# Kernel tuning notes

Measured on AMD Instinct MI355X. Metric: run time of the kernel, lower is better.

The kernel has to match this reference:

```python
import jax, jax.numpy as jnp
import numpy as np

N = 50000
H = 256
EPS = 1e-5

def setup_inputs() -> dict:
    key = jax.random.key(0)
    ks = jax.random.split(key, 8)
    d = 128
    inp = {
        'x': jax.random.normal(ks[0], (N, d), jnp.float32),
        'edge_index': jax.random.randint(ks[1], (2, 800000), 0, N, jnp.int64),
        'W1': jax.random.normal(ks[2], (d, H), jnp.float32) * (2.0 / d) ** 0.5,
        'b1': jnp.zeros((H,), jnp.float32),
        'g1': jnp.ones((H,), jnp.float32),
        'be1': jnp.zeros((H,), jnp.float32),
        'W2': jax.random.normal(ks[3], (H, H), jnp.float32) * (2.0 / H) ** 0.5,
        'b2': jnp.zeros((H,), jnp.float32),
        'g2': jnp.ones((H,), jnp.float32),
        'be2': jnp.zeros((H,), jnp.float32),
        'W3': jax.random.normal(ks[4], (H, H), jnp.float32) * (2.0 / H) ** 0.5,
        'b3': jnp.zeros((H,), jnp.float32),
        'g3': jnp.ones((H,), jnp.float32),
        'be3': jnp.zeros((H,), jnp.float32),
        'Wf1': jax.random.normal(ks[5], (H, H // 2), jnp.float32) * (2.0 / H) ** 0.5,
        'bf1': jnp.zeros((H // 2,), jnp.float32),
        'Wf2': jax.random.normal(ks[6], (H // 2, 1), jnp.float32) * (2.0 / (H // 2)) ** 0.5,
        'bf2': jnp.zeros((1,), jnp.float32),
    }
    return inp

def _gcn_norm(edge_index):
    # add self-loops, symmetric normalization (PyG GCNConv defaults)
    loop = jnp.arange(N, dtype=edge_index.dtype)
    row = jnp.concatenate([edge_index[0], loop])  # source
    col = jnp.concatenate([edge_index[1], loop])  # target
    deg = jax.ops.segment_sum(jnp.ones_like(col, jnp.float32), col, num_segments=N)
    dis = jnp.where(deg > 0, jax.lax.rsqrt(deg), 0.0)
    norm = dis[row] * dis[col]  # [E+N]
    return row, col, norm

def _conv(x, W, b, row, col, norm):
    xw = x @ W                       # [N,H]
    msg = xw[row] * norm[:, None]    # gather + scale, [E+N,H]
    out = jax.ops.segment_sum(msg, col, num_segments=N)
    return out + b

def _ln(x, g, b):
    mu = jnp.mean(x, axis=-1, keepdims=True)
    var = jnp.var(x, axis=-1, keepdims=True)
    return (x - mu) * jax.lax.rsqrt(var + EPS) * g + b

def reference(x, edge_index, W1, b1, g1, be1, W2, b2, g2, be2, W3, b3, g3, be3, Wf1, bf1, Wf2, bf2):
    row, col, norm = _gcn_norm(edge_index)
    x1 = jax.nn.relu(_ln(_conv(x, W1, b1, row, col, norm), g1, be1))
    x2 = jax.nn.relu(_ln(_conv(x1, W2, b2, row, col, norm), g2, be2)) + 0.7 * x1
    x3 = jax.nn.relu(_ln(_conv(x2, W3, b3, row, col, norm), g3, be3)) * 0.7 + x2
    h = jax.nn.relu(x3 @ Wf1 + bf1)
    return h @ Wf2 + bf2  # [N,1]
```

## Files before the change

### kernel.cpp

```cpp
#include <hip/hip_runtime.h>
#include <cstdint>
#include <cstddef>

#define HDIM 256
#define DIN 128
#define EPSV 1e-5f
#define SCHUNK 1024

typedef __attribute__((ext_vector_type(8))) short short8;
typedef __attribute__((ext_vector_type(4))) float f32x4;

__device__ __forceinline__ float bf2f(unsigned int u16) {
  union { unsigned int i; float f; } v; v.i = u16 << 16; return v.f;
}
__device__ __forceinline__ unsigned short f2bf(float f) {
  union { float f; unsigned int i; } v; v.f = f;
  unsigned int u = v.i;
  return (unsigned short)((u + 0x7fffu + ((u >> 16) & 1u)) >> 16);
}
__device__ __forceinline__ float4 ldbf4(const unsigned short* p) {
  uint2 v = *(const uint2*)p;
  return make_float4(bf2f(v.x & 0xffffu), bf2f(v.x >> 16),
                     bf2f(v.y & 0xffffu), bf2f(v.y >> 16));
}
__device__ __forceinline__ void stbf4(unsigned short* p, float a, float b, float c, float d) {
  uint2 o;
  o.x = (unsigned int)f2bf(a) | ((unsigned int)f2bf(b) << 16);
  o.y = (unsigned int)f2bf(c) | ((unsigned int)f2bf(d) << 16);
  *(uint2*)p = o;
}
#define ACC8(u) do { \
    acc[0] += bf2f((u).x & 0xffffu); acc[1] += bf2f((u).x >> 16); \
    acc[2] += bf2f((u).y & 0xffffu); acc[3] += bf2f((u).y >> 16); \
    acc[4] += bf2f((u).z & 0xffffu); acc[5] += bf2f((u).z >> 16); \
    acc[6] += bf2f((u).w & 0xffffu); acc[7] += bf2f((u).w >> 16); } while (0)

__global__ __launch_bounds__(256) void hist_k(const int* __restrict__ col, int* deg, int e) {
  int i = blockIdx.x * 256 + threadIdx.x;
  if (i < e) atomicAdd(&deg[col[i]], 1);
}

__global__ __launch_bounds__(256) void scanA_k(const int* __restrict__ deg,
                                               int* __restrict__ row_ptr,
                                               int* __restrict__ blockSums,
                                               float* __restrict__ dis, int n) {
  __shared__ int waveSums[4];
  const int tid = threadIdx.x, lane = tid & 63, w = tid >> 6;
  const int base = blockIdx.x * SCHUNK + tid * 4;
  int v0 = 0, v1 = 0, v2 = 0, v3 = 0;
  if (base + 0 < n) v0 = deg[base + 0];
  if (base + 1 < n) v1 = deg[base + 1];
  if (base + 2 < n) v2 = deg[base + 2];
  if (base + 3 < n) v3 = deg[base + 3];
  if (base + 0 < n) dis[base + 0] = rsqrtf((float)(v0 + 1));
  if (base + 1 < n) dis[base + 1] = rsqrtf((float)(v1 + 1));
  if (base + 2 < n) dis[base + 2] = rsqrtf((float)(v2 + 1));
  if (base + 3 < n) dis[base + 3] = rsqrtf((float)(v3 + 1));
  int tsum = v0 + v1 + v2 + v3;
  int inc = tsum;
#pragma unroll
  for (int off = 1; off < 64; off <<= 1) {
    int t = __shfl_up(inc, off);
    if (lane >= off) inc += t;
  }
  if (lane == 63) waveSums[w] = inc;
  __syncthreads();
  int woff = 0;
#pragma unroll
  for (int k = 0; k < 4; ++k) woff += (k < w) ? waveSums[k] : 0;
  int excl = woff + inc - tsum;
  if (base + 0 < n) row_ptr[base + 0] = excl;
  if (base + 1 < n) row_ptr[base + 1] = excl + v0;
  if (base + 2 < n) row_ptr[base + 2] = excl + v0 + v1;
  if (base + 3 < n) row_ptr[base + 3] = excl + v0 + v1 + v2;
  if (tid == 255) blockSums[blockIdx.x] = woff + inc;
}

__global__ __launch_bounds__(256) void scanC_k(int* __restrict__ row_ptr,
                                               const int* __restrict__ bsums,
                                               int n, int e, int nbs) {
  __shared__ int s_add;
  if (threadIdx.x < 64) {
    int v = (threadIdx.x < nbs && threadIdx.x < blockIdx.x) ? bsums[threadIdx.x] : 0;
#pragma unroll
    for (int off = 1; off < 64; off <<= 1) v += __shfl_xor(v, off);
    if (threadIdx.x == 0) s_add = v;
  }
  __syncthreads();
  const int add = s_add;
  const int base = blockIdx.x * SCHUNK + threadIdx.x * 4;
#pragma unroll
  for (int k = 0; k < 4; ++k)
    if (base + k < n) row_ptr[base + k] += add;
  if (blockIdx.x == 0 && threadIdx.x == 0) row_ptr[n] = e;
}

__global__ __launch_bounds__(256) void fill_k(const int* __restrict__ row,
                                              const int* __restrict__ col,
                                              const int* __restrict__ row_ptr,
                                              int* cur, int* srcs, int e) {
  int i = blockIdx.x * 256 + threadIdx.x;
  if (i < e) {
    int c = col[i];
    int p = row_ptr[c] + atomicAdd(&cur[c], 1);
    srcs[p] = row[i];
  }
}

__device__ __forceinline__ void packW(const float* __restrict__ W,
                                      unsigned short* __restrict__ out,
                                      int idx, int C) {
  int j = idx & 7, lane = (idx >> 3) & 63, rest = idx >> 9;
  int NSUB = C >> 4;
  int ns = rest % NSUB, kb = rest / NSUB;
  int k = kb * 32 + (lane >> 4) * 8 + j;
  int c = ns * 16 + (lane & 15);
  out[idx] = f2bf(W[(size_t)k * C + c]);
}

__global__ __launch_bounds__(256) void prep_k(
    const float* __restrict__ W1, const float* __restrict__ W2,
    const float* __restrict__ W3, const float* __restrict__ Wf1,
    const float* __restrict__ x, const float* __restrict__ dis,
    unsigned short* __restrict__ W1p, unsigned short* __restrict__ W2p,
    unsigned short* __restrict__ W3p, unsigned short* __restrict__ Wf1p,
    unsigned short* __restrict__ xs, int nx) {
  int idx = blockIdx.x * 256 + threadIdx.x;
  const int s0 = DIN * HDIM, s1 = s0 + HDIM * HDIM, s2 = s1 + HDIM * HDIM,
            s3 = s2 + HDIM * 128;
  if (idx < s0) packW(W1, W1p, idx, HDIM);
  else if (idx < s1) packW(W2, W2p, idx - s0, HDIM);
  else if (idx < s2) packW(W3, W3p, idx - s1, HDIM);
  else if (idx < s3) packW(Wf1, Wf1p, idx - s2, 128);
  else {
    int o = idx - s3;
    if (o < nx) xs[o] = f2bf(x[o] * dis[o >> 7]);
  }
}

template<int MODE, int K, bool SOUT>
__global__ __launch_bounds__(512) void fused_k(
    const unsigned short* __restrict__ xs, const int* __restrict__ row_ptr,
    const int* __restrict__ srcs, const float* __restrict__ dis,
    const unsigned short* __restrict__ Wp,
    const float* __restrict__ bias, const float* __restrict__ gam,
    const float* __restrict__ bet, const unsigned short* __restrict__ xprev,
    unsigned short* __restrict__ out, int n) {
  constexpr int CN = 256, NSUB = 16, KC = K / 32;
  constexpr int STRIDE = K + 8;
  constexpr int LPR = K / 8;
  constexpr int RP = 64 / LPR;
  constexpr int NIT = 8 / RP;
  __shared__ unsigned short aggS[64 * STRIDE];
  __shared__ float red_s[64][4], red_q[64][4];

  const int t = threadIdx.x;
  const int w = t >> 6, lane = t & 63;
  const int m0 = blockIdx.x * 64;

  {
    const int gi = lane / LPR, li = lane % LPR;
    const unsigned short* xb = xs + li * 8;
#pragma unroll
    for (int it = 0; it < NIT; ++it) {
      const int lr = w * 8 + it * RP + gi;
      const int tg = m0 + lr;
      const int tgc = tg < n ? tg : n - 1;
      const int beg = row_ptr[tgc], end = row_ptr[tgc + 1];
      const float di = dis[tgc];
      float acc[8];
      {
        uint4 v = *(const uint4*)(xb + (size_t)tgc * K);
        acc[0] = bf2f(v.x & 0xffffu); acc[1] = bf2f(v.x >> 16);
        acc[2] = bf2f(v.y & 0xffffu); acc[3] = bf2f(v.y >> 16);
        acc[4] = bf2f(v.z & 0xffffu); acc[5] = bf2f(v.z >> 16);
        acc[6] = bf2f(v.w & 0xffffu); acc[7] = bf2f(v.w >> 16);
      }
      int j = beg;
      for (; j + 16 <= end; j += 16) {
        int4 sA = *(const int4*)(srcs + j);
        int4 sB = *(const int4*)(srcs + j + 4);
        int4 sC = *(const int4*)(srcs + j + 8);
        int4 sD = *(const int4*)(srcs + j + 12);
        uint4 u0 = *(const uint4*)(xb + (size_t)sA.x * K);
        uint4 u1 = *(const uint4*)(xb + (size_t)sA.y * K);
        uint4 u2 = *(const uint4*)(xb + (size_t)sA.z * K);
        uint4 u3 = *(const uint4*)(xb + (size_t)sA.w * K);
        uint4 u4 = *(const uint4*)(xb + (size_t)sB.x * K);
        uint4 u5 = *(const uint4*)(xb + (size_t)sB.y * K);
        uint4 u6 = *(const uint4*)(xb + (size_t)sB.z * K);
        uint4 u7 = *(const uint4*)(xb + (size_t)sB.w * K);
        uint4 u8 = *(const uint4*)(xb + (size_t)sC.x * K);
        uint4 u9 = *(const uint4*)(xb + (size_t)sC.y * K);
        uint4 uA = *(const uint4*)(xb + (size_t)sC.z * K);
        uint4 uB = *(const uint4*)(xb + (size_t)sC.w * K);
        uint4 uC = *(const uint4*)(xb + (size_t)sD.x * K);
        uint4 uD = *(const uint4*)(xb + (size_t)sD.y * K);
        uint4 uE = *(const uint4*)(xb + (size_t)sD.z * K);
        uint4 uF = *(const uint4*)(xb + (size_t)sD.w * K);
        ACC8(u0); ACC8(u1); ACC8(u2); ACC8(u3);
        ACC8(u4); ACC8(u5); ACC8(u6); ACC8(u7);
        ACC8(u8); ACC8(u9); ACC8(uA); ACC8(uB);
        ACC8(uC); ACC8(uD); ACC8(uE); ACC8(uF);
      }
      for (; j + 4 <= end; j += 4) {
        int4 sA = *(const int4*)(srcs + j);
        uint4 u0 = *(const uint4*)(xb + (size_t)sA.x * K);
        uint4 u1 = *(const uint4*)(xb + (size_t)sA.y * K);
        uint4 u2 = *(const uint4*)(xb + (size_t)sA.z * K);
        uint4 u3 = *(const uint4*)(xb + (size_t)sA.w * K);
        ACC8(u0); ACC8(u1); ACC8(u2); ACC8(u3);
      }
      for (; j < end; ++j) {
        uint4 u = *(const uint4*)(xb + (size_t)srcs[j] * K);
        ACC8(u);
      }
      uint4 o;
      o.x = (unsigned int)f2bf(di * acc[0]) | ((unsigned int)f2bf(di * acc[1]) << 16);
      o.y = (unsigned int)f2bf(di * acc[2]) | ((unsigned int)f2bf(di * acc[3]) << 16);
      o.z = (unsigned int)f2bf(di * acc[4]) | ((unsigned int)f2bf(di * acc[5]) << 16);
      o.w = (unsigned int)f2bf(di * acc[6]) | ((unsigned int)f2bf(di * acc[7]) << 16);
      *(uint4*)&aggS[lr * STRIDE + li * 8] = o;
    }
  }
  __syncthreads();

  const int rg = w & 1, cg = w >> 1;
  const int gq = lane >> 4, i = lane & 15;
  const unsigned short* aL0 = &aggS[(rg * 32 + i) * STRIDE + gq * 8];
  const unsigned short* aL1 = aL0 + 16 * STRIDE;
  const short8* wp = (const short8*)Wp + (size_t)(cg * 4) * 64 + lane;

  f32x4 acc[2][4];
#pragma unroll
  for (int rr = 0; rr < 2; ++rr)
#pragma unroll
    for (int j = 0; j < 4; ++j) acc[rr][j] = (f32x4){0.f, 0.f, 0.f, 0.f};

  short8 wf[4];
#pragma unroll
  for (int j = 0; j < 4; ++j) wf[j] = wp[j * 64];

#pragma unroll
  for (int kc = 0; kc < KC; ++kc) {
    short8 nwf[4];
    if (kc + 1 < KC) {
#pragma unroll
      for (int j = 0; j < 4; ++j) nwf[j] = wp[(size_t)(kc + 1) * NSUB * 64 + j * 64];
    }
    short8 af0 = *(const short8*)(aL0 + kc * 32);
    short8 af1 = *(const short8*)(aL1 + kc * 32);
#pragma unroll
    for (int j = 0; j < 4; ++j) {
      acc[0][j] = __builtin_amdgcn_mfma_f32_16x16x32_bf16(wf[j], af0, acc[0][j], 0, 0, 0);
      acc[1][j] = __builtin_amdgcn_mfma_f32_16x16x32_bf16(wf[j], af1, acc[1][j], 0, 0, 0);
    }
    if (kc + 1 < KC) {
#pragma unroll
      for (int j = 0; j < 4; ++j) wf[j] = nwf[j];
    }
  }

  const int colb = cg * 64 + gq * 4;
  float s0 = 0.f, q0 = 0.f, s1 = 0.f, q1 = 0.f;
#pragma unroll
  for (int j = 0; j < 4; ++j) {
    f32x4 b4 = *(const f32x4*)(bias + colb + j * 16);
#pragma unroll
    for (int r = 0; r < 4; ++r) {
      acc[0][j][r] += b4[r];
      acc[1][j][r] += b4[r];
      float v = acc[0][j][r]; s0 += v; q0 += v * v;
      float u = acc[1][j][r]; s1 += u; q1 += u * u;
    }
  }
  s0 += __shfl_xor(s0, 16); s0 += __shfl_xor(s0, 32);
  q0 += __shfl_xor(q0, 16); q0 += __shfl_xor(q0, 32);
  s1 += __shfl_xor(s1, 16); s1 += __shfl_xor(s1, 32);
  q1 += __shfl_xor(q1, 16); q1 += __shfl_xor(q1, 32);
  if (gq == 0) {
    red_s[rg * 32 + i][cg] = s0;      red_q[rg * 32 + i][cg] = q0;
    red_s[rg * 32 + 16 + i][cg] = s1; red_q[rg * 32 + 16 + i][cg] = q1;
  }
  __syncthreads();

#pragma unroll
  for (int rr = 0; rr < 2; ++rr) {
    int il = rg * 32 + rr * 16 + i;
    int r = m0 + il;
    if (r >= n) continue;
    float ss = (red_s[il][0] + red_s[il][1]) + (red_s[il][2] + red_s[il][3]);
    float qq = (red_q[il][0] + red_q[il][1]) + (red_q[il][2] + red_q[il][3]);
    float mu = ss * (1.f / CN);
    float inv = rsqrtf(qq * (1.f / CN) - mu * mu + EPSV);
    float di = dis[r];
    float rinv = (MODE != 0) ? 1.0f / di : 0.f;
    unsigned short* op = out + (size_t)r * CN + colb;
    const unsigned short* pp = (MODE != 0) ? (xprev + (size_t)r * CN + colb) : nullptr;
#pragma unroll
    for (int j = 0; j < 4; ++j) {
      f32x4 g4 = *(const f32x4*)(gam + colb + j * 16);
      f32x4 e4 = *(const f32x4*)(bet + colb + j * 16);
      float o0 = fmaxf((acc[rr][j][0] - mu) * inv * g4[0] + e4[0], 0.f);
      float o1 = fmaxf((acc[rr][j][1] - mu) * inv * g4[1] + e4[1], 0.f);
      float o2 = fmaxf((acc[rr][j][2] - mu) * inv * g4[2] + e4[2], 0.f);
      float o3 = fmaxf((acc[rr][j][3] - mu) * inv * g4[3] + e4[3], 0.f);
      if (MODE == 1) {
        float4 pv = ldbf4(pp + j * 16);
        o0 += 0.7f * rinv * pv.x; o1 += 0.7f * rinv * pv.y;
        o2 += 0.7f * rinv * pv.z; o3 += 0.7f * rinv * pv.w;
      } else if (MODE == 2) {
        float4 pv = ldbf4(pp + j * 16);
        o0 = o0 * 0.7f + rinv * pv.x; o1 = o1 * 0.7f + rinv * pv.y;
        o2 = o2 * 0.7f + rinv * pv.z; o3 = o3 * 0.7f + rinv * pv.w;
      }
      if (SOUT) { o0 *= di; o1 *= di; o2 *= di; o3 *= di; }
      stbf4(op + j * 16, o0, o1, o2, o3);
    }
  }
}

__global__ __launch_bounds__(256) void gemmdot_k(
    const unsigned short* __restrict__ A, const unsigned short* __restrict__ Wp,
    const float* __restrict__ b1, const float* __restrict__ w2,
    const float* __restrict__ b2, float* __restrict__ out, int n) {
  constexpr int K = 256, NSUB = 8, KC = 8;
  __shared__ float redh[64][2];
  const int t = threadIdx.x;
  const int w = t >> 6, lane = t & 63;
  const int rg = w & 1, cg = w >> 1;
  const int gq = lane >> 4, i = lane & 15;
  const int m0 = blockIdx.x * 64;
  const int r0 = m0 + rg * 32 + i, r1 = r0 + 16;
  const int l0 = r0 < n ? r0 : n - 1, l1 = r1 < n ? r1 : n - 1;
  const unsigned short* a0 = A + (size_t)l0 * K + gq * 8;
  const unsigned short* a1 = A + (size_t)l1 * K + gq * 8;
  const short8* wp = (const short8*)Wp + (size_t)(cg * 4) * 64 + lane;

  f32x4 acc[2][4];
#pragma unroll
  for (int rr = 0; rr < 2; ++rr)
#pragma unroll
    for (int j = 0; j < 4; ++j) acc[rr][j] = (f32x4){0.f, 0.f, 0.f, 0.f};

  short8 af0 = *(const short8*)a0;
  short8 af1 = *(const short8*)a1;
  short8 wf[4];
#pragma unroll
  for (int j = 0; j < 4; ++j) wf[j] = wp[j * 64];

#pragma unroll
  for (int kc = 0; kc < KC; ++kc) {
    short8 naf0, naf1, nwf[4];
    if (kc + 1 < KC) {
      naf0 = *(const short8*)(a0 + (kc + 1) * 32);
      naf1 = *(const short8*)(a1 + (kc + 1) * 32);
#pragma unroll
      for (int j = 0; j < 4; ++j) nwf[j] = wp[(size_t)(kc + 1) * NSUB * 64 + j * 64];
    }
#pragma unroll
    for (int j = 0; j < 4; ++j) {
      acc[0][j] = __builtin_amdgcn_mfma_f32_16x16x32_bf16(wf[j], af0, acc[0][j], 0, 0, 0);
      acc[1][j] = __builtin_amdgcn_mfma_f32_16x16x32_bf16(wf[j], af1, acc[1][j], 0, 0, 0);
    }
    if (kc + 1 < KC) {
      af0 = naf0; af1 = naf1;
#pragma unroll
      for (int j = 0; j < 4; ++j) wf[j] = nwf[j];
    }
  }

  const int colb = cg * 64 + gq * 4;
  float p0 = 0.f, p1 = 0.f;
#pragma unroll
  for (int j = 0; j < 4; ++j) {
    f32x4 bb = *(const f32x4*)(b1 + colb + j * 16);
    f32x4 ww = *(const f32x4*)(w2 + colb + j * 16);
#pragma unroll
    for (int r = 0; r < 4; ++r) {
      p0 += fmaxf(acc[0][j][r] + bb[r], 0.f) * ww[r];
      p1 += fmaxf(acc[1][j][r] + bb[r], 0.f) * ww[r];
    }
  }
  p0 += __shfl_xor(p0, 16); p0 += __shfl_xor(p0, 32);
  p1 += __shfl_xor(p1, 16); p1 += __shfl_xor(p1, 32);
  if (gq == 0) {
    redh[rg * 32 + i][cg] = p0;
    redh[rg * 32 + 16 + i][cg] = p1;
  }
  __syncthreads();
  if (t < 64) {
    int r = m0 + t;
    if (r < n) out[r] = redh[t][0] + redh[t][1] + b2[0];
  }
}

extern "C" void kernel_launch(void* const* d_in, const int* in_sizes, int n_in,
                              void* d_out, int out_size, void* d_ws, size_t ws_size,
                              hipStream_t stream) {
  const float* x   = (const float*)d_in[0];
  const int*   ei  = (const int*)d_in[1];
  const float* W1  = (const float*)d_in[2];
  const float* b1  = (const float*)d_in[3];
  const float* g1  = (const float*)d_in[4];
  const float* be1 = (const float*)d_in[5];
  const float* W2  = (const float*)d_in[6];
  const float* b2  = (const float*)d_in[7];
  const float* g2  = (const float*)d_in[8];
  const float* be2 = (const float*)d_in[9];
  const float* W3  = (const float*)d_in[10];
  const float* b3  = (const float*)d_in[11];
  const float* g3  = (const float*)d_in[12];
  const float* be3 = (const float*)d_in[13];
  const float* Wf1 = (const float*)d_in[14];
  const float* bf1 = (const float*)d_in[15];
  const float* Wf2 = (const float*)d_in[16];
  const float* bf2 = (const float*)d_in[17];
  float* out = (float*)d_out;

  const int n = in_sizes[0] / DIN;
  const int e = in_sizes[1] / 2;
  const int* row = ei;
  const int* col = ei + e;

  char* ws = (char*)d_ws;
  size_t off = 0;
  auto alloc = [&](size_t bytes) -> void* {
    void* p = ws + off;
    off = (off + bytes + 255) & ~(size_t)255;
    return p;
  };
  float*          dis     = (float*)alloc((size_t)n * 4);
  int*            deg_i   = (int*)alloc((size_t)n * 4);
  int*            cur     = (int*)alloc((size_t)n * 4);
  int*            row_ptr = (int*)alloc((size_t)(n + 1) * 4);
  int*            bsums   = (int*)alloc((size_t)256 * 4);
  int*            srcs    = (int*)alloc((size_t)e * 4);
  unsigned short* W1p     = (unsigned short*)alloc((size_t)DIN * HDIM * 2);
  unsigned short* W2p     = (unsigned short*)alloc((size_t)HDIM * HDIM * 2);
  unsigned short* W3p     = (unsigned short*)alloc((size_t)HDIM * HDIM * 2);
  unsigned short* Wf1p    = (unsigned short*)alloc((size_t)HDIM * 128 * 2);
  unsigned short* xsb     = (unsigned short*)alloc((size_t)n * DIN * 2);
  unsigned short* x1s     = (unsigned short*)alloc((size_t)n * HDIM * 2);
  unsigned short* x2s     = (unsigned short*)alloc((size_t)n * HDIM * 2);
  unsigned short* x3      = (unsigned short*)alloc((size_t)n * HDIM * 2);

  const int eb  = (e + 255) / 256;
  const int gb  = (n + 63) / 64;
  const int sb_ = (n + SCHUNK - 1) / SCHUNK;
  const int prep_tot = DIN * HDIM + HDIM * HDIM + HDIM * HDIM + HDIM * 128 + n * DIN;

  hipMemsetAsync(deg_i, 0, ((char*)row_ptr - (char*)deg_i), stream);
  hist_k<<<eb, 256, 0, stream>>>(col, deg_i, e);
  scanA_k<<<sb_, 256, 0, stream>>>(deg_i, row_ptr, bsums, dis, n);
  scanC_k<<<sb_, 256, 0, stream>>>(row_ptr, bsums, n, e, sb_);
  fill_k<<<eb, 256, 0, stream>>>(row, col, row_ptr, cur, srcs, e);

  prep_k<<<(prep_tot + 255) / 256, 256, 0, stream>>>(W1, W2, W3, Wf1, x, dis,
                                                     W1p, W2p, W3p, Wf1p, xsb, n * DIN);

  fused_k<0, DIN, true><<<gb, 512, 0, stream>>>(
      xsb, row_ptr, srcs, dis, W1p, b1, g1, be1, nullptr, x1s, n);

  fused_k<1, HDIM, true><<<gb, 512, 0, stream>>>(
      x1s, row_ptr, srcs, dis, W2p, b2, g2, be2, x1s, x2s, n);

  fused_k<2, HDIM, false><<<gb, 512, 0, stream>>>(
      x2s, row_ptr, srcs, dis, W3p, b3, g3, be3, x2s, x3, n);

  gemmdot_k<<<gb, 256, 0, stream>>>(x3, Wf1p, bf1, Wf2, bf2, out, n);
}
```

Measured before the change: 480.4 us.

## Split GCN layers into gather and MFMA roles overlapped across half-graph launches

Each fused layer becomes two roles, an aggregation (gather) role that writes bf16 aggregates to a global buffer and a GEMM+LayerNorm role working on 128-row tiles. Rows are split into two halves and three launches are issued per layer, so gathering the second half runs alongside the GEMM on the first half. The aim is to overlap the memory-bound gather with MFMA work and to make GEMM tiles wider. CSR fill now reuses per-edge ranks from the histogram atomics instead of a second atomic pass, and the final GEMM-dot kernel moves to 512 threads and 128 rows per block. This costs a global round-trip for the aggregates, extra launches, and a larger workspace.

```diff
diff --git a/kernel.cpp b/kernel.cpp
--- a/kernel.cpp
+++ b/kernel.cpp
@@ -35,9 +35,10 @@
     acc[4] += bf2f((u).z & 0xffffu); acc[5] += bf2f((u).z >> 16); \
     acc[6] += bf2f((u).w & 0xffffu); acc[7] += bf2f((u).w >> 16); } while (0)
 
-__global__ __launch_bounds__(256) void hist_k(const int* __restrict__ col, int* deg, int e) {
+__global__ __launch_bounds__(256) void hist_k(const int* __restrict__ col,
+                                              int* deg, int* __restrict__ rank, int e) {
   int i = blockIdx.x * 256 + threadIdx.x;
-  if (i < e) atomicAdd(&deg[col[i]], 1);
+  if (i < e) rank[i] = atomicAdd(&deg[col[i]], 1);
 }
 
 __global__ __launch_bounds__(256) void scanA_k(const int* __restrict__ deg,
@@ -98,13 +99,10 @@
 __global__ __launch_bounds__(256) void fill_k(const int* __restrict__ row,
                                               const int* __restrict__ col,
                                               const int* __restrict__ row_ptr,
-                                              int* cur, int* srcs, int e) {
+                                              const int* __restrict__ rank,
+                                              int* __restrict__ srcs, int e) {
   int i = blockIdx.x * 256 + threadIdx.x;
-  if (i < e) {
-    int c = col[i];
-    int p = row_ptr[c] + atomicAdd(&cur[c], 1);
-    srcs[p] = row[i];
-  }
+  if (i < e) srcs[row_ptr[col[i]] + rank[i]] = row[i];
 }
 
 __device__ __forceinline__ void packW(const float* __restrict__ W,
@@ -139,132 +137,137 @@
 }
 
 template<int MODE, int K, bool SOUT>
-__global__ __launch_bounds__(512) void fused_k(
+__global__ __launch_bounds__(512) void combo_k(
     const unsigned short* __restrict__ xs, const int* __restrict__ row_ptr,
     const int* __restrict__ srcs, const float* __restrict__ dis,
-    const unsigned short* __restrict__ Wp,
+    unsigned short* __restrict__ agg, const unsigned short* __restrict__ Wp,
     const float* __restrict__ bias, const float* __restrict__ gam,
     const float* __restrict__ bet, const unsigned short* __restrict__ xprev,
-    unsigned short* __restrict__ out, int n) {
-  constexpr int CN = 256, NSUB = 16, KC = K / 32;
-  constexpr int STRIDE = K + 8;
-  constexpr int LPR = K / 8;
-  constexpr int RP = 64 / LPR;
-  constexpr int NIT = 8 / RP;
-  __shared__ unsigned short aggS[64 * STRIDE];
-  __shared__ float red_s[64][4], red_q[64][4];
-
+    unsigned short* __restrict__ out,
+    int Gb, int gRow0, int gEnd, int Lb, int lRow0, int lEnd, int n) {
+  constexpr int CN = 256, NSUBT = 16, KC = K / 32;
+  constexpr int LPR = K / 8, RPW = 64 / LPR, RPB = 8 * RPW;
+  __shared__ float red_s[128][2], red_q[128][2];
+  int b = blockIdx.x, role, sub;
+  int mm = 2 * (Gb < Lb ? Gb : Lb);
+  if (b < mm) { role = b & 1; sub = b >> 1; }
+  else { sub = (mm >> 1) + (b - mm); role = (Gb > Lb) ? 0 : 1; }
   const int t = threadIdx.x;
   const int w = t >> 6, lane = t & 63;
-  const int m0 = blockIdx.x * 64;
-
-  {
-    const int gi = lane / LPR, li = lane % LPR;
-    const unsigned short* xb = xs + li * 8;
-#pragma unroll
-    for (int it = 0; it < NIT; ++it) {
-      const int lr = w * 8 + it * RP + gi;
-      const int tg = m0 + lr;
-      const int tgc = tg < n ? tg : n - 1;
-      const int beg = row_ptr[tgc], end = row_ptr[tgc + 1];
-      const float di = dis[tgc];
-      float acc[8];
-      {
-        uint4 v = *(const uint4*)(xb + (size_t)tgc * K);
-        acc[0] = bf2f(v.x & 0xffffu); acc[1] = bf2f(v.x >> 16);
-        acc[2] = bf2f(v.y & 0xffffu); acc[3] = bf2f(v.y >> 16);
-        acc[4] = bf2f(v.z & 0xffffu); acc[5] = bf2f(v.z >> 16);
-        acc[6] = bf2f(v.w & 0xffffu); acc[7] = bf2f(v.w >> 16);
-      }
-      int j = beg;
-      for (; j + 16 <= end; j += 16) {
-        int4 sA = *(const int4*)(srcs + j);
-        int4 sB = *(const int4*)(srcs + j + 4);
-        int4 sC = *(const int4*)(srcs + j + 8);
-        int4 sD = *(const int4*)(srcs + j + 12);
-        uint4 u0 = *(const uint4*)(xb + (size_t)sA.x * K);
-        uint4 u1 = *(const uint4*)(xb + (size_t)sA.y * K);
-        uint4 u2 = *(const uint4*)(xb + (size_t)sA.z * K);
-        uint4 u3 = *(const uint4*)(xb + (size_t)sA.w * K);
-        uint4 u4 = *(const uint4*)(xb + (size_t)sB.x * K);
-        uint4 u5 = *(const uint4*)(xb + (size_t)sB.y * K);
-        uint4 u6 = *(const uint4*)(xb + (size_t)sB.z * K);
-        uint4 u7 = *(const uint4*)(xb + (size_t)sB.w * K);
-        uint4 u8 = *(const uint4*)(xb + (size_t)sC.x * K);
-        uint4 u9 = *(const uint4*)(xb + (size_t)sC.y * K);
-        uint4 uA = *(const uint4*)(xb + (size_t)sC.z * K);
-        uint4 uB = *(const uint4*)(xb + (size_t)sC.w * K);
-        uint4 uC = *(const uint4*)(xb + (size_t)sD.x * K);
-        uint4 uD = *(const uint4*)(xb + (size_t)sD.y * K);
-        uint4 uE = *(const uint4*)(xb + (size_t)sD.z * K);
-        uint4 uF = *(const uint4*)(xb + (size_t)sD.w * K);
-        ACC8(u0); ACC8(u1); ACC8(u2); ACC8(u3);
-        ACC8(u4); ACC8(u5); ACC8(u6); ACC8(u7);
-        ACC8(u8); ACC8(u9); ACC8(uA); ACC8(uB);
-        ACC8(uC); ACC8(uD); ACC8(uE); ACC8(uF);
-      }
-      for (; j + 4 <= end; j += 4) {
-        int4 sA = *(const int4*)(srcs + j);
-        uint4 u0 = *(const uint4*)(xb + (size_t)sA.x * K);
-        uint4 u1 = *(const uint4*)(xb + (size_t)sA.y * K);
-        uint4 u2 = *(const uint4*)(xb + (size_t)sA.z * K);
-        uint4 u3 = *(const uint4*)(xb + (size_t)sA.w * K);
-        ACC8(u0); ACC8(u1); ACC8(u2); ACC8(u3);
-      }
-      for (; j < end; ++j) {
-        uint4 u = *(const uint4*)(xb + (size_t)srcs[j] * K);
-        ACC8(u);
-      }
+
+  if (role == 0) {
+    const int rsub = lane / LPR, li = lane % LPR;
+    const int i = gRow0 + sub * RPB + w * RPW + rsub;
+    bool valid = i < gEnd;
+    int ic = valid ? i : n - 1;
+    int beg = row_ptr[ic], end = row_ptr[ic + 1];
+    float di = dis[ic];
+    const int co = li * 8;
+    const unsigned short* xb = xs + co;
+    float acc[8];
+    {
+      uint4 v = *(const uint4*)(xb + (size_t)ic * K);
+      acc[0] = bf2f(v.x & 0xffffu); acc[1] = bf2f(v.x >> 16);
+      acc[2] = bf2f(v.y & 0xffffu); acc[3] = bf2f(v.y >> 16);
+      acc[4] = bf2f(v.z & 0xffffu); acc[5] = bf2f(v.z >> 16);
+      acc[6] = bf2f(v.w & 0xffffu); acc[7] = bf2f(v.w >> 16);
+    }
+    int j = beg;
+    for (; j + 16 <= end; j += 16) {
+      int4 sA = *(const int4*)(srcs + j);
+      int4 sB = *(const int4*)(srcs + j + 4);
+      int4 sC = *(const int4*)(srcs + j + 8);
+      int4 sD = *(const int4*)(srcs + j + 12);
+      uint4 u0 = *(const uint4*)(xb + (size_t)sA.x * K);
+      uint4 u1 = *(const uint4*)(xb + (size_t)sA.y * K);
+      uint4 u2 = *(const uint4*)(xb + (size_t)sA.z * K);
+      uint4 u3 = *(const uint4*)(xb + (size_t)sA.w * K);
+      uint4 u4 = *(const uint4*)(xb + (size_t)sB.x * K);
+      uint4 u5 = *(const uint4*)(xb + (size_t)sB.y * K);
+      uint4 u6 = *(const uint4*)(xb + (size_t)sB.z * K);
+      uint4 u7 = *(const uint4*)(xb + (size_t)sB.w * K);
+      uint4 u8 = *(const uint4*)(xb + (size_t)sC.x * K);
+      uint4 u9 = *(const uint4*)(xb + (size_t)sC.y * K);
+      uint4 uA = *(const uint4*)(xb + (size_t)sC.z * K);
+      uint4 uB = *(const uint4*)(xb + (size_t)sC.w * K);
+      uint4 uC = *(const uint4*)(xb + (size_t)sD.x * K);
+      uint4 uD = *(const uint4*)(xb + (size_t)sD.y * K);
+      uint4 uE = *(const uint4*)(xb + (size_t)sD.z * K);
+      uint4 uF = *(const uint4*)(xb + (size_t)sD.w * K);
+      ACC8(u0); ACC8(u1); ACC8(u2); ACC8(u3);
+      ACC8(u4); ACC8(u5); ACC8(u6); ACC8(u7);
+      ACC8(u8); ACC8(u9); ACC8(uA); ACC8(uB);
+      ACC8(uC); ACC8(uD); ACC8(uE); ACC8(uF);
+    }
+    for (; j + 4 <= end; j += 4) {
+      int4 sA = *(const int4*)(srcs + j);
+      uint4 u0 = *(const uint4*)(xb + (size_t)sA.x * K);
+      uint4 u1 = *(const uint4*)(xb + (size_t)sA.y * K);
+      uint4 u2 = *(const uint4*)(xb + (size_t)sA.z * K);
+      uint4 u3 = *(const uint4*)(xb + (size_t)sA.w * K);
+      ACC8(u0); ACC8(u1); ACC8(u2); ACC8(u3);
+    }
+    for (; j < end; ++j) {
+      uint4 u = *(const uint4*)(xb + (size_t)srcs[j] * K);
+      ACC8(u);
+    }
+    if (valid) {
       uint4 o;
       o.x = (unsigned int)f2bf(di * acc[0]) | ((unsigned int)f2bf(di * acc[1]) << 16);
       o.y = (unsigned int)f2bf(di * acc[2]) | ((unsigned int)f2bf(di * acc[3]) << 16);
       o.z = (unsigned int)f2bf(di * acc[4]) | ((unsigned int)f2bf(di * acc[5]) << 16);
       o.w = (unsigned int)f2bf(di * acc[6]) | ((unsigned int)f2bf(di * acc[7]) << 16);
-      *(uint4*)&aggS[lr * STRIDE + li * 8] = o;
-    }
-  }
-  __syncthreads();
-
-  const int rg = w & 1, cg = w >> 1;
+      *(uint4*)(agg + (size_t)i * K + co) = o;
+    }
+    return;
+  }
+
+  const int rg = w & 3, cg = w >> 2;
   const int gq = lane >> 4, i = lane & 15;
-  const unsigned short* aL0 = &aggS[(rg * 32 + i) * STRIDE + gq * 8];
-  const unsigned short* aL1 = aL0 + 16 * STRIDE;
-  const short8* wp = (const short8*)Wp + (size_t)(cg * 4) * 64 + lane;
-
-  f32x4 acc[2][4];
+  const int m0 = lRow0 + sub * 128;
+  const int r0 = m0 + rg * 32 + i, r1 = r0 + 16;
+  const int l0 = r0 < n ? r0 : n - 1, l1 = r1 < n ? r1 : n - 1;
+  const unsigned short* a0 = agg + (size_t)l0 * K + gq * 8;
+  const unsigned short* a1 = agg + (size_t)l1 * K + gq * 8;
+  const short8* wp = (const short8*)Wp + (size_t)(cg * 8) * 64 + lane;
+
+  f32x4 acc[2][8];
 #pragma unroll
   for (int rr = 0; rr < 2; ++rr)
 #pragma unroll
-    for (int j = 0; j < 4; ++j) acc[rr][j] = (f32x4){0.f, 0.f, 0.f, 0.f};
-
-  short8 wf[4];
-#pragma unroll
-  for (int j = 0; j < 4; ++j) wf[j] = wp[j * 64];
+    for (int j = 0; j < 8; ++j) acc[rr][j] = (f32x4){0.f, 0.f, 0.f, 0.f};
+
+  short8 af0 = *(const short8*)a0;
+  short8 af1 = *(const short8*)a1;
+  short8 wf[8];
+#pragma unroll
+  for (int j = 0; j < 8; ++j) wf[j] = wp[j * 64];
 
 #pragma unroll
   for (int kc = 0; kc < KC; ++kc) {
-    short8 nwf[4];
+    short8 naf0, naf1, nwf[8];
     if (kc + 1 < KC) {
-#pragma unroll
-      for (int j = 0; j < 4; ++j) nwf[j] = wp[(size_t)(kc + 1) * NSUB * 64 + j * 64];
-    }
-    short8 af0 = *(const short8*)(aL0 + kc * 32);
-    short8 af1 = *(const short8*)(aL1 + kc * 32);
-#pragma unroll
-    for (int j = 0; j < 4; ++j) {
+      naf0 = *(const short8*)(a0 + (kc + 1) * 32);
+      naf1 = *(const short8*)(a1 + (kc + 1) * 32);
+#pragma unroll
+      for (int j = 0; j < 8; ++j) nwf[j] = wp[(size_t)(kc + 1) * NSUBT * 64 + j * 64];
+    }
+#pragma unroll
+    for (int j = 0; j < 8; ++j) {
       acc[0][j] = __builtin_amdgcn_mfma_f32_16x16x32_bf16(wf[j], af0, acc[0][j], 0, 0, 0);
       acc[1][j] = __builtin_amdgcn_mfma_f32_16x16x32_bf16(wf[j], af1, acc[1][j], 0, 0, 0);
     }
     if (kc + 1 < KC) {
-#pragma unroll
-      for (int j = 0; j < 4; ++j) wf[j] = nwf[j];
-    }
-  }
-
-  const int colb = cg * 64 + gq * 4;
+      af0 = naf0; af1 = naf1;
+#pragma unroll
+      for (int j = 0; j < 8; ++j) wf[j] = nwf[j];
+    }
+  }
+
+  const int colb = cg * 128 + gq * 4;
   float s0 = 0.f, q0 = 0.f, s1 = 0.f, q1 = 0.f;
 #pragma unroll
-  for (int j = 0; j < 4; ++j) {
+  for (int j = 0; j < 8; ++j) {
     f32x4 b4 = *(const f32x4*)(bias + colb + j * 16);
 #pragma unroll
     for (int r = 0; r < 4; ++r) {
@@ -288,9 +291,9 @@
   for (int rr = 0; rr < 2; ++rr) {
     int il = rg * 32 + rr * 16 + i;
     int r = m0 + il;
-    if (r >= n) continue;
-    float ss = (red_s[il][0] + red_s[il][1]) + (red_s[il][2] + red_s[il][3]);
-    float qq = (red_q[il][0] + red_q[il][1]) + (red_q[il][2] + red_q[il][3]);
+    if (r >= lEnd) continue;
+    float ss = red_s[il][0] + red_s[il][1];
+    float qq = red_q[il][0] + red_q[il][1];
     float mu = ss * (1.f / CN);
     float inv = rsqrtf(qq * (1.f / CN) - mu * mu + EPSV);
     float di = dis[r];
@@ -298,7 +301,7 @@
     unsigned short* op = out + (size_t)r * CN + colb;
     const unsigned short* pp = (MODE != 0) ? (xprev + (size_t)r * CN + colb) : nullptr;
 #pragma unroll
-    for (int j = 0; j < 4; ++j) {
+    for (int j = 0; j < 8; ++j) {
       f32x4 g4 = *(const f32x4*)(gam + colb + j * 16);
       f32x4 e4 = *(const f32x4*)(bet + colb + j * 16);
       float o0 = fmaxf((acc[rr][j][0] - mu) * inv * g4[0] + e4[0], 0.f);
@@ -320,17 +323,17 @@
   }
 }
 
-__global__ __launch_bounds__(256) void gemmdot_k(
+__global__ __launch_bounds__(512) void gemmdot_k(
     const unsigned short* __restrict__ A, const unsigned short* __restrict__ Wp,
     const float* __restrict__ b1, const float* __restrict__ w2,
     const float* __restrict__ b2, float* __restrict__ out, int n) {
-  constexpr int K = 256, NSUB = 8, KC = 8;
-  __shared__ float redh[64][2];
+  constexpr int K = 256, NSUBT = 8, KC = 8;
+  __shared__ float redh[128][2];
   const int t = threadIdx.x;
   const int w = t >> 6, lane = t & 63;
-  const int rg = w & 1, cg = w >> 1;
+  const int rg = w & 3, cg = w >> 2;
   const int gq = lane >> 4, i = lane & 15;
-  const int m0 = blockIdx.x * 64;
+  const int m0 = blockIdx.x * 128;
   const int r0 = m0 + rg * 32 + i, r1 = r0 + 16;
   const int l0 = r0 < n ? r0 : n - 1, l1 = r1 < n ? r1 : n - 1;
   const unsigned short* a0 = A + (size_t)l0 * K + gq * 8;
@@ -356,7 +359,7 @@
       naf0 = *(const short8*)(a0 + (kc + 1) * 32);
       naf1 = *(const short8*)(a1 + (kc + 1) * 32);
 #pragma unroll
-      for (int j = 0; j < 4; ++j) nwf[j] = wp[(size_t)(kc + 1) * NSUB * 64 + j * 64];
+      for (int j = 0; j < 4; ++j) nwf[j] = wp[(size_t)(kc + 1) * NSUBT * 64 + j * 64];
     }
 #pragma unroll
     for (int j = 0; j < 4; ++j) {
@@ -389,7 +392,7 @@
     redh[rg * 32 + 16 + i][cg] = p1;
   }
   __syncthreads();
-  if (t < 64) {
+  if (t < 128) {
     int r = m0 + t;
     if (r < n) out[r] = redh[t][0] + redh[t][1] + b2[0];
   }
@@ -432,41 +435,71 @@
   };
   float*          dis     = (float*)alloc((size_t)n * 4);
   int*            deg_i   = (int*)alloc((size_t)n * 4);
-  int*            cur     = (int*)alloc((size_t)n * 4);
   int*            row_ptr = (int*)alloc((size_t)(n + 1) * 4);
   int*            bsums   = (int*)alloc((size_t)256 * 4);
+  int*            rank    = (int*)alloc((size_t)e * 4);
   int*            srcs    = (int*)alloc((size_t)e * 4);
   unsigned short* W1p     = (unsigned short*)alloc((size_t)DIN * HDIM * 2);
   unsigned short* W2p     = (unsigned short*)alloc((size_t)HDIM * HDIM * 2);
   unsigned short* W3p     = (unsigned short*)alloc((size_t)HDIM * HDIM * 2);
   unsigned short* Wf1p    = (unsigned short*)alloc((size_t)HDIM * 128 * 2);
   unsigned short* xsb     = (unsigned short*)alloc((size_t)n * DIN * 2);
+  unsigned short* agg     = (unsigned short*)alloc((size_t)n * HDIM * 2);
   unsigned short* x1s     = (unsigned short*)alloc((size_t)n * HDIM * 2);
   unsigned short* x2s     = (unsigned short*)alloc((size_t)n * HDIM * 2);
-  unsigned short* x3      = (unsigned short*)alloc((size_t)n * HDIM * 2);
+  unsigned short* a1      = agg;
+  unsigned short* x3      = x1s;
 
   const int eb  = (e + 255) / 256;
-  const int gb  = (n + 63) / 64;
+  const int gb  = (n + 127) / 128;
   const int sb_ = (n + SCHUNK - 1) / SCHUNK;
   const int prep_tot = DIN * HDIM + HDIM * HDIM + HDIM * HDIM + HDIM * 128 + n * DIN;
 
-  hipMemsetAsync(deg_i, 0, ((char*)row_ptr - (char*)deg_i), stream);
-  hist_k<<<eb, 256, 0, stream>>>(col, deg_i, e);
+  int nA = ((n + 255) / 256) * 128;
+  if (nA > n) nA = n;
+  const int nB = n - nA;
+  const int LbA = (nA + 127) / 128, LbB = (nB + 127) / 128;
+  const int GbA1 = (nA + 31) / 32, GbB1 = (nB + 31) / 32;
+  const int GbA2 = (nA + 15) / 16, GbB2 = (nB + 15) / 16;
+
+  hipMemsetAsync(deg_i, 0, (size_t)n * 4, stream);
+  hist_k<<<eb, 256, 0, stream>>>(col, deg_i, rank, e);
   scanA_k<<<sb_, 256, 0, stream>>>(deg_i, row_ptr, bsums, dis, n);
   scanC_k<<<sb_, 256, 0, stream>>>(row_ptr, bsums, n, e, sb_);
-  fill_k<<<eb, 256, 0, stream>>>(row, col, row_ptr, cur, srcs, e);
+  fill_k<<<eb, 256, 0, stream>>>(row, col, row_ptr, rank, srcs, e);
 
   prep_k<<<(prep_tot + 255) / 256, 256, 0, stream>>>(W1, W2, W3, Wf1, x, dis,
                                                      W1p, W2p, W3p, Wf1p, xsb, n * DIN);
 
-  fused_k<0, DIN, true><<<gb, 512, 0, stream>>>(
-      xsb, row_ptr, srcs, dis, W1p, b1, g1, be1, nullptr, x1s, n);
-
-  fused_k<1, HDIM, true><<<gb, 512, 0, stream>>>(
-      x1s, row_ptr, srcs, dis, W2p, b2, g2, be2, x1s, x2s, n);
-
-  fused_k<2, HDIM, false><<<gb, 512, 0, stream>>>(
-      x2s, row_ptr, srcs, dis, W3p, b3, g3, be3, x2s, x3, n);
-
-  gemmdot_k<<<gb, 256, 0, stream>>>(x3, Wf1p, bf1, Wf2, bf2, out, n);
-}
+  combo_k<0, DIN, true><<<GbA1, 512, 0, stream>>>(
+      xsb, row_ptr, srcs, dis, a1, W1p, b1, g1, be1, nullptr, x1s,
+      GbA1, 0, nA, 0, 0, 0, n);
+  combo_k<0, DIN, true><<<GbB1 + LbA, 512, 0, stream>>>(
+      xsb, row_ptr, srcs, dis, a1, W1p, b1, g1, be1, nullptr, x1s,
+      GbB1, nA, n, LbA, 0, nA, n);
+  combo_k<0, DIN, true><<<LbB, 512, 0, stream>>>(
+      xsb, row_ptr, srcs, dis, a1, W1p, b1, g1, be1, nullptr, x1s,
+      0, 0, 0, LbB, nA, n, n);
+
+  combo_k<1, HDIM, true><<<GbA2, 512, 0, stream>>>(
+      x1s, row_ptr, srcs, dis, agg, W2p, b2, g2, be2, x1s, x2s,
+      GbA2, 0, nA, 0, 0, 0, n);
+  combo_k<1, HDIM, true><<<GbB2 + LbA, 512, 0, stream>>>(
+      x1s, row_ptr, srcs, dis, agg, W2p, b2, g2, be2, x1s, x2s,
+      GbB2, nA, n, LbA, 0, nA, n);
+  combo_k<1, HDIM, true><<<LbB, 512, 0, stream>>>(
+      x1s, row_ptr, srcs, dis, agg, W2p, b2, g2, be2, x1s, x2s,
+      0, 0, 0, LbB, nA, n, n);
+
+  combo_k<2, HDIM, false><<<GbA2, 512, 0, stream>>>(
+      x2s, row_ptr, srcs, dis, agg, W3p, b3, g3, be3, x2s, x3,
+      GbA2, 0, nA, 0, 0, 0, n);
+  combo_k<2, HDIM, false><<<GbB2 + LbA, 512, 0, stream>>>(
+      x2s, row_ptr, srcs, dis, agg, W3p, b3, g3, be3, x2s, x3,
+      GbB2, nA, n, LbA, 0, nA, n);
+  combo_k<2, HDIM, false><<<LbB, 512, 0, stream>>>(
+      x2s, row_ptr, srcs, dis, agg, W3p, b3, g3, be3, x2s, x3,
+      0, 0, 0, LbB, nA, n, n);
+
+  gemmdot_k<<<gb, 512, 0, stream>>>(x3, Wf1p, bf1, Wf2, bf2, out, n);
+}
```

Result: slower. 527.0 us (+9.7%).
